# Performance work log

Hardware: AMD Instinct MI355X
Metric: run time of the kernel (lower is better)

Reference implementation:

```python
import jax, jax.numpy as jnp
import numpy as np

EMB_D, N_SLOTS, KEY_D, N_ITER = 768, 8, 128, 5
ATTN_EPS = 1e-8
LN_EPS = 1e-5


def layer_norm(x, g, b):
    mu = jnp.mean(x, axis=-1, keepdims=True)
    var = jnp.mean(jnp.square(x - mu), axis=-1, keepdims=True)
    return (x - mu) * jax.lax.rsqrt(var + LN_EPS) * g + b


def xavier(key, shape):
    fan_in, fan_out = shape[-1], shape[-2] if len(shape) > 1 else shape[-1]
    a = float(np.sqrt(6.0 / (fan_in + fan_out)))
    return jax.random.uniform(key, shape, jnp.float32, -a, a)


def setup_inputs() -> dict:
    key = jax.random.key(0)
    ks = jax.random.split(key, 24)
    B, N = 128, 196
    k = KEY_D
    inp = {
        "features": jax.random.normal(ks[0], (B, N, EMB_D), jnp.float32),
        "slot_noise": jax.random.normal(ks[1], (B, N_SLOTS, k), jnp.float32),
        # LayerNorms
        "ln_in_g": jnp.ones((EMB_D,), jnp.float32), "ln_in_b": jnp.zeros((EMB_D,), jnp.float32),
        "ln_slot_g": jnp.ones((k,), jnp.float32), "ln_slot_b": jnp.zeros((k,), jnp.float32),
        "ln_out_g": jnp.ones((k,), jnp.float32), "ln_out_b": jnp.zeros((k,), jnp.float32),
        "ln_dec_g": jnp.ones((k,), jnp.float32), "ln_dec_b": jnp.zeros((k,), jnp.float32),
        # slot prior
        "mu": xavier(ks[2], (1, 1, k)),
        "log_sigma": xavier(ks[3], (1, 1, k)),
        # projections (torch Linear weight layout: [out, in])
        "Wk": xavier(ks[4], (k, EMB_D)),
        "Wq": xavier(ks[5], (k, k)),
        "Wv": xavier(ks[6], (k, EMB_D)),
        # GRUCell
        "W_ih": jax.random.uniform(ks[7], (3 * k, k), jnp.float32, -1.0/np.sqrt(k), 1.0/np.sqrt(k)),
        "W_hh": jax.random.uniform(ks[8], (3 * k, k), jnp.float32, -1.0/np.sqrt(k), 1.0/np.sqrt(k)),
        "b_ih": jnp.zeros((3 * k,), jnp.float32),
        "b_hh": jnp.zeros((3 * k,), jnp.float32),
        # slot MLP
        "mlp_W1": xavier(ks[9], (k, k)), "mlp_b1": jnp.zeros((k,), jnp.float32),
        "mlp_W2": xavier(ks[10], (k, k)), "mlp_b2": jnp.zeros((k,), jnp.float32),
        # decoder
        "dec_W1": xavier(ks[11], (2 * k, k)), "dec_b1": jnp.zeros((2 * k,), jnp.float32),
        "dec_W2": xavier(ks[12], (EMB_D, 2 * k)), "dec_b2": jnp.zeros((EMB_D,), jnp.float32),
        "dec_W3": xavier(ks[13], (EMB_D, EMB_D)), "dec_b3": jnp.zeros((EMB_D,), jnp.float32),
    }
    return inp


def gru_cell(x, h, W_ih, W_hh, b_ih, b_hh):
    gi = x @ W_ih.T + b_ih  # [*, 3k]
    gh = h @ W_hh.T + b_hh
    ir, iz, inn = jnp.split(gi, 3, axis=-1)
    hr, hz, hn = jnp.split(gh, 3, axis=-1)
    r = jax.nn.sigmoid(ir + hr)
    z = jax.nn.sigmoid(iz + hz)
    n = jnp.tanh(inn + r * hn)
    return (1.0 - z) * n + z * h


def reference(features, slot_noise, ln_in_g, ln_in_b, ln_slot_g, ln_slot_b,
              ln_out_g, ln_out_b, ln_dec_g, ln_dec_b, mu, log_sigma,
              Wk, Wq, Wv, W_ih, W_hh, b_ih, b_hh,
              mlp_W1, mlp_b1, mlp_W2, mlp_b2,
              dec_W1, dec_b1, dec_W2, dec_b2, dec_W3, dec_b3):
    feats_ln = layer_norm(features, ln_in_g, ln_in_b)  # [B,N,E]
    slots = slot_noise * jnp.exp(log_sigma) + mu       # [B,K,D]
    k_proj = (feats_ln @ Wk.T) * (KEY_D ** -0.5)       # [B,N,D]
    v_proj = feats_ln @ Wv.T                           # [B,N,D]

    attn_vis = None
    for _ in range(N_ITER):
        slots_prev = slots
        s_ln = layer_norm(slots, ln_slot_g, ln_slot_b)
        q = s_ln @ Wq.T                                # [B,K,D]
        logits = jnp.einsum('bnd,bkd->bnk', k_proj, q)
        attn_vis = jax.nn.softmax(logits, axis=-1)     # softmax over slots
        attn = attn_vis + ATTN_EPS
        attn = attn / jnp.sum(attn, axis=-2, keepdims=True)  # normalize over tokens
        updates = jnp.einsum('bnk,bnd->bkd', attn, v_proj)
        slots = gru_cell(updates, slots_prev, W_ih, W_hh, b_ih, b_hh)
        h = jax.nn.relu(layer_norm(slots, ln_out_g, ln_out_b) @ mlp_W1.T + mlp_b1)
        slots = slots + (h @ mlp_W2.T + mlp_b2)

    sf = layer_norm(slots, ln_dec_g, ln_dec_b)
    sf = jax.nn.relu(sf @ dec_W1.T + dec_b1)
    sf = jax.nn.relu(sf @ dec_W2.T + dec_b2)
    sf = sf @ dec_W3.T + dec_b3                        # [B,K,E]
    recon = jnp.einsum('bkd,bnk->bnd', sf, attn_vis)   # [B,N,E]
    recon_loss = jnp.mean(jnp.square(recon - features))
    return slots, attn_vis, recon_loss
```

## Files before the change

kernel.cpp:

```cpp
#include <hip/hip_runtime.h>
#include <hip/hip_bf16.h>
#include <math.h>

#define B_    128
#define N_    196
#define E_    768
#define K_    8
#define D_    128
#define BNR   (B_*N_)
#define ITERS 5

#define OFF_PART   0
#define OFF_SDEC   512
#define OFF_WBF    66048
#define OFF_KPBF   639488
#define OFF_VPTBF  2343424
#define OFF_ABF    4178432

typedef __attribute__((ext_vector_type(8))) short bf16x8;
typedef __attribute__((ext_vector_type(4))) float f32x4;

#define MFMA16(a, b, c) __builtin_amdgcn_mfma_f32_16x16x32_bf16(a, b, c, 0, 0, 0)

__device__ __forceinline__ float wave_red_sum64(float v) {
    #pragma unroll
    for (int o = 32; o > 0; o >>= 1) v += __shfl_xor(v, o);
    return v;
}

__device__ __forceinline__ unsigned short f2bf(float v) {
    union { float f; unsigned int u; } c; c.f = v;
    unsigned int u = c.u + 0x7fffu + ((c.u >> 16) & 1u);
    return (unsigned short)(u >> 16);
}

__device__ __forceinline__ void gl_lds16(const void* g, void* l) {
    __builtin_amdgcn_global_load_lds(
        (const __attribute__((address_space(1))) unsigned int*)g,
        (__attribute__((address_space(3))) unsigned int*)l, 16, 0, 0);
}

__device__ __forceinline__ int swz128(int row, int j) {
    return row * 128 + ((((j >> 3) ^ (row & 7))) << 3) + (j & 7);
}
__device__ __forceinline__ int swz256(int row, int j) {
    return row * 256 + ((((j >> 3) ^ (row & 7))) << 3) + (j & 7);
}
__device__ __forceinline__ bf16x8 ldA128(const unsigned short* base, int row, int kq, int ks) {
    int ch = (ks * 4 + kq) ^ (row & 7);
    return *(const bf16x8*)(base + row * 128 + ch * 8);
}
__device__ __forceinline__ bf16x8 ldA256(const unsigned short* base, int row, int kq, int ks) {
    int ch = (ks * 4 + kq) ^ (row & 7);
    return *(const bf16x8*)(base + row * 256 + ch * 8);
}
__device__ __forceinline__ bf16x8 ldW128(const unsigned short* W, int row, int ks, int kq) {
    return *(const bf16x8*)(W + (size_t)row * 128 + ks * 32 + kq * 8);
}

__global__ __launch_bounds__(256) void wfold_k(const float* __restrict__ Wq,
                                               const float* __restrict__ Wk,
                                               unsigned short* __restrict__ WMt) {
    __shared__ __align__(16) unsigned short Aq[128 * 128];
    __shared__ __align__(16) unsigned short Bk[128 * 128];
    const float s = 0.08838834764831845f;
    int t = threadIdx.x;
    int e0 = blockIdx.x * 128;
    for (int idx = t; idx < 16384; idx += 256) {
        int o = idx >> 7, c = idx & 127;
        Aq[swz128(c, o)] = f2bf(Wq[(size_t)o * 128 + c]);
        Bk[swz128(c, o)] = f2bf(Wk[(size_t)o * 768 + e0 + c] * s);
    }
    __syncthreads();
    int w = t >> 6, l = t & 63;
    int wr = w >> 1, wc = w & 1, fr = l & 15, kq = l >> 4;
    f32x4 acc[4][4];
    #pragma unroll
    for (int mi = 0; mi < 4; ++mi)
        #pragma unroll
        for (int nj = 0; nj < 4; ++nj) acc[mi][nj] = (f32x4){0.f, 0.f, 0.f, 0.f};
    #pragma unroll
    for (int ks = 0; ks < 4; ++ks) {
        bf16x8 af[4], bfr[4];
        #pragma unroll
        for (int mi = 0; mi < 4; ++mi) af[mi] = ldA128(Aq, wr * 64 + mi * 16 + fr, kq, ks);
        #pragma unroll
        for (int nj = 0; nj < 4; ++nj) bfr[nj] = ldA128(Bk, wc * 64 + nj * 16 + fr, kq, ks);
        #pragma unroll
        for (int mi = 0; mi < 4; ++mi)
            #pragma unroll
            for (int nj = 0; nj < 4; ++nj)
                acc[mi][nj] = MFMA16(af[mi], bfr[nj], acc[mi][nj]);
    }
    #pragma unroll
    for (int mi = 0; mi < 4; ++mi) {
        int rowbase = wr * 64 + mi * 16 + kq * 4;
        #pragma unroll
        for (int nj = 0; nj < 4; ++nj) {
            int col = e0 + wc * 64 + nj * 16 + fr;
            #pragma unroll
            for (int r = 0; r < 4; ++r)
                WMt[(size_t)(rowbase + r) * 768 + col] = f2bf(acc[mi][nj][r]);
        }
    }
}

struct WCEnt { const float* s; unsigned short* d; int t0; };
struct WCArgs { WCEnt m[8]; };

__global__ __launch_bounds__(256) void wprep_k(WCArgs a,
                                               unsigned short* __restrict__ kpb,
                                               unsigned short* __restrict__ vpt) {
    int bid = blockIdx.x;
    if (bid < 512) {
        int i = 0;
        #pragma unroll
        for (int j = 1; j < 8; ++j) if (bid >= a.m[j].t0) i = j;
        int off = (bid - a.m[i].t0) * 2048 + threadIdx.x * 8;
        const float* s = a.m[i].s + off;
        unsigned short* d = a.m[i].d + off;
        float4 v0 = *(const float4*)s, v1 = *(const float4*)(s + 4);
        ushort4 o0, o1;
        o0.x = f2bf(v0.x); o0.y = f2bf(v0.y); o0.z = f2bf(v0.z); o0.w = f2bf(v0.w);
        o1.x = f2bf(v1.x); o1.y = f2bf(v1.y); o1.z = f2bf(v1.z); o1.w = f2bf(v1.w);
        *(ushort4*)d = o0; *(ushort4*)(d + 4) = o1;
    } else {
        int i = (bid - 512) * 256 + threadIdx.x;
        ushort4 z = {0, 0, 0, 0};
        if (i < 49152) {
            int q = i * 4;
            int b = q / 1536, off = q - b * 1536;
            *(ushort4*)(kpb + ((size_t)b * 208 + 196) * 128 + off) = z;
        } else {
            int c = i - 49152;
            int bd = c / 7, cc = c - bd * 7;
            *(ushort4*)(vpt + (size_t)bd * 224 + 196 + cc * 4) = z;
        }
    }
}

__global__ __launch_bounds__(256) void ln_bf16_k(const float* __restrict__ f,
                                                 const float* __restrict__ g,
                                                 const float* __restrict__ bv,
                                                 unsigned short* __restrict__ out) {
    int wid = blockIdx.x * 4 + (threadIdx.x >> 6);
    int lane = threadIdx.x & 63;
    const float* row = f + (size_t)wid * E_;
    float4 x[3];
    float s = 0.f, s2 = 0.f;
    #pragma unroll
    for (int c = 0; c < 3; ++c) {
        x[c] = *(const float4*)(row + c * 256 + lane * 4);
        s  += x[c].x + x[c].y + x[c].z + x[c].w;
        s2 += x[c].x * x[c].x + x[c].y * x[c].y + x[c].z * x[c].z + x[c].w * x[c].w;
    }
    s  = wave_red_sum64(s);
    s2 = wave_red_sum64(s2);
    float m = s * (1.f / E_);
    float rs = rsqrtf(s2 * (1.f / E_) - m * m + 1e-5f);
    #pragma unroll
    for (int c = 0; c < 3; ++c) {
        float4 g4 = *(const float4*)(g + c * 256 + lane * 4);
        float4 b4 = *(const float4*)(bv + c * 256 + lane * 4);
        ushort4 o;
        o.x = f2bf((x[c].x - m) * rs * g4.x + b4.x);
        o.y = f2bf((x[c].y - m) * rs * g4.y + b4.y);
        o.z = f2bf((x[c].z - m) * rs * g4.z + b4.z);
        o.w = f2bf((x[c].w - m) * rs * g4.w + b4.w);
        *(ushort4*)(out + (size_t)wid * E_ + c * 256 + lane * 4) = o;
    }
}

__global__ __launch_bounds__(512) void mfma_proj_k(const unsigned short* __restrict__ Abf,
                                                   const unsigned short* __restrict__ WMt,
                                                   const unsigned short* __restrict__ Wv_bf,
                                                   unsigned short* __restrict__ kpq_bf,
                                                   unsigned short* __restrict__ vpT_bf) {
    __shared__ __align__(16) unsigned short As[128 * 64];
    __shared__ __align__(16) unsigned short Bs[256 * 64];
    const int t = threadIdx.x, w = t >> 6, l = t & 63;
    const int m0 = blockIdx.x * 128;
    const int wr = w >> 2, wc = w & 3;
    const int fr = l & 15, kq = l >> 4;
    f32x4 acc[4][4];
    #pragma unroll
    for (int mi = 0; mi < 4; ++mi)
        #pragma unroll
        for (int nj = 0; nj < 4; ++nj) acc[mi][nj] = (f32x4){0.f, 0.f, 0.f, 0.f};

    for (int ks = 0; ks < E_; ks += 64) {
        __syncthreads();
        #pragma unroll
        for (int j = 0; j < 2; ++j) {
            int ci = j * 512 + (w << 6) + l;
            int r = ci >> 3, c = ci & 7, cg = c ^ (r & 7);
            gl_lds16(Abf + (size_t)(m0 + r) * E_ + ks + cg * 8,
                     As + (size_t)(j * 512 + (w << 6)) * 8);
        }
        #pragma unroll
        for (int j = 0; j < 4; ++j) {
            int ci = j * 512 + (w << 6) + l;
            int r = ci >> 3, c = ci & 7, cg = c ^ (r & 7);
            const unsigned short* src = (r < 128)
                ? WMt   + (size_t)r * E_ + ks + cg * 8
                : Wv_bf + (size_t)(r - 128) * E_ + ks + cg * 8;
            gl_lds16(src, Bs + (size_t)(j * 512 + (w << 6)) * 8);
        }
        __syncthreads();
        #pragma unroll
        for (int kk = 0; kk < 2; ++kk) {
            bf16x8 af[4], bfr[4];
            #pragma unroll
            for (int mi = 0; mi < 4; ++mi) {
                int rr = wr * 64 + mi * 16 + fr;
                af[mi] = *(const bf16x8*)(As + rr * 64 + (((kk * 4 + kq) ^ (rr & 7))) * 8);
            }
            #pragma unroll
            for (int nj = 0; nj < 4; ++nj) {
                int rr = wc * 64 + nj * 16 + fr;
                bfr[nj] = *(const bf16x8*)(Bs + rr * 64 + (((kk * 4 + kq) ^ (rr & 7))) * 8);
            }
            #pragma unroll
            for (int mi = 0; mi < 4; ++mi)
                #pragma unroll
                for (int nj = 0; nj < 4; ++nj)
                    acc[mi][nj] = MFMA16(af[mi], bfr[nj], acc[mi][nj]);
        }
    }
    __syncthreads();
    if (wc < 2) {
        #pragma unroll
        for (int mi = 0; mi < 4; ++mi) {
            int rowbase = m0 + wr * 64 + mi * 16 + kq * 4;
            #pragma unroll
            for (int r = 0; r < 4; ++r) {
                int m = rowbase + r;
                int b = m / 196, rr = m - b * 196;
                size_t o = ((size_t)b * 208 + rr) * 128;
                #pragma unroll
                for (int nj = 0; nj < 4; ++nj)
                    kpq_bf[o + wc * 64 + nj * 16 + fr] = f2bf(acc[mi][nj][r]);
            }
        }
    } else {
        int dbase = (wc - 2) * 64;
        #pragma unroll
        for (int mi = 0; mi < 4; ++mi) {
            int tok = wr * 64 + mi * 16 + kq * 4;
            #pragma unroll
            for (int nj = 0; nj < 4; ++nj) {
                int d = dbase + nj * 16 + fr;
                ushort4 pk;
                pk.x = f2bf(acc[mi][nj][0]); pk.y = f2bf(acc[mi][nj][1]);
                pk.z = f2bf(acc[mi][nj][2]); pk.w = f2bf(acc[mi][nj][3]);
                *(ushort4*)(Bs + d * 128 + (tok ^ ((d & 7) << 3))) = pk;
            }
        }
    }
    __syncthreads();
    {
        int d = t >> 2, mg = t & 3;
        #pragma unroll
        for (int sc = 0; sc < 4; ++sc) {
            int mstart = mg * 32 + sc * 8;
            int cm = mstart >> 3;
            const unsigned short* src = Bs + d * 128 + ((cm ^ (d & 7)) << 3);
            int g0 = m0 + mstart;
            int b0 = g0 / 196, rr0 = g0 - b0 * 196;
            int b7 = (g0 + 7) / 196;
            if (b0 == b7) {
                unsigned short* dst = vpT_bf + ((size_t)b0 * 128 + d) * 224 + rr0;
                *(ushort4*)(dst)     = *(const ushort4*)(src);
                *(ushort4*)(dst + 4) = *(const ushort4*)(src + 4);
            } else {
                #pragma unroll
                for (int e = 0; e < 8; ++e) {
                    int g = g0 + e;
                    int bb = g / 196, rr = g - bb * 196;
                    vpT_bf[((size_t)bb * 128 + d) * 224 + rr] = src[e];
                }
            }
        }
    }
}

template<int KTOT, int EPI>
__global__ __launch_bounds__(256) void mfma_mlp_k(const unsigned short* __restrict__ A,
                                                  const unsigned short* __restrict__ Bw,
                                                  const float* __restrict__ bias,
                                                  unsigned short* __restrict__ out_bf,
                                                  float* __restrict__ out_f,
                                                  int ldN) {
    __shared__ __align__(16) unsigned short As[128 * 64];
    __shared__ __align__(16) unsigned short Bs[128 * 64];
    const int t = threadIdx.x, w = t >> 6, l = t & 63;
    const int m0 = blockIdx.x * 128;
    const int n0 = blockIdx.y * 128;
    const int wr = w >> 1, wc = w & 1;
    const int fr = l & 15, kq = l >> 4;
    f32x4 acc[4][4];
    #pragma unroll
    for (int mi = 0; mi < 4; ++mi)
        #pragma unroll
        for (int nj = 0; nj < 4; ++nj) acc[mi][nj] = (f32x4){0.f, 0.f, 0.f, 0.f};

    for (int ks = 0; ks < KTOT; ks += 64) {
        __syncthreads();
        #pragma unroll
        for (int j = 0; j < 4; ++j) {
            int ci = (w << 8) + (j << 6) + l;
            int r = ci >> 3, c = ci & 7;
            int cg = c ^ (r & 7);
            gl_lds16(A  + (size_t)(m0 + r) * KTOT + ks + cg * 8,
                     As + (size_t)((w << 8) + (j << 6)) * 8);
            gl_lds16(Bw + (size_t)(n0 + r) * KTOT + ks + cg * 8,
                     Bs + (size_t)((w << 8) + (j << 6)) * 8);
        }
        __syncthreads();
        #pragma unroll
        for (int kk = 0; kk < 2; ++kk) {
            bf16x8 af[4], bfr[4];
            int ch = (kk * 4 + kq) ^ (fr & 7);
            #pragma unroll
            for (int mi = 0; mi < 4; ++mi)
                af[mi] = *(const bf16x8*)(As + (wr * 64 + mi * 16 + fr) * 64 + ch * 8);
            #pragma unroll
            for (int nj = 0; nj < 4; ++nj)
                bfr[nj] = *(const bf16x8*)(Bs + (wc * 64 + nj * 16 + fr) * 64 + ch * 8);
            #pragma unroll
            for (int mi = 0; mi < 4; ++mi)
                #pragma unroll
                for (int nj = 0; nj < 4; ++nj)
                    acc[mi][nj] = MFMA16(af[mi], bfr[nj], acc[mi][nj]);
        }
    }
    #pragma unroll
    for (int mi = 0; mi < 4; ++mi) {
        int rowbase = m0 + wr * 64 + mi * 16 + kq * 4;
        #pragma unroll
        for (int nj = 0; nj < 4; ++nj) {
            int col = n0 + wc * 64 + nj * 16 + fr;
            float bc = bias[col];
            #pragma unroll
            for (int r = 0; r < 4; ++r) {
                float v = acc[mi][nj][r] + bc;
                if (EPI == 0)
                    out_bf[(size_t)(rowbase + r) * ldN + col] = f2bf(fmaxf(v, 0.f));
                else
                    out_f[(size_t)(rowbase + r) * ldN + col] = v;
            }
        }
    }
}

__global__ __launch_bounds__(512) void slot_iter_mfma(
    const float* __restrict__ noise,
    const float* __restrict__ lsg, const float* __restrict__ lsb,
    const float* __restrict__ log_, const float* __restrict__ lob,
    const float* __restrict__ ldg_, const float* __restrict__ ldb_,
    const float* __restrict__ mup, const float* __restrict__ lsig,
    const unsigned short* __restrict__ Wih_bf,
    const unsigned short* __restrict__ Whh_bf,
    const float* __restrict__ bih, const float* __restrict__ bhh,
    const unsigned short* __restrict__ W1_bf, const float* __restrict__ mb1,
    const unsigned short* __restrict__ W2_bf, const float* __restrict__ mb2,
    const unsigned short* __restrict__ kpq_bf,
    const unsigned short* __restrict__ vpT_bf,
    float* __restrict__ out_slots, float* __restrict__ out_attn,
    unsigned short* __restrict__ sdec_bf) {

    __shared__ float slots[8][128];
    __shared__ float attn[208][9];
    __shared__ float colpart[8][8];
    __shared__ __align__(16) unsigned short sln_bf[2048];
    __shared__ __align__(16) unsigned short upd_bf[2048];
    __shared__ __align__(16) unsigned short slots_bf[2048];
    __shared__ __align__(16) unsigned short h_bf[2048];
    __shared__ __align__(16) unsigned short attnT_bf[4096];

    const int b = blockIdx.x, t = threadIdx.x;
    const int lane = t & 63, w = t >> 6;
    const int fr = lane & 15, kq = lane >> 4;

    for (int i = t; i < 2048; i += 512) {
        sln_bf[i] = 0; upd_bf[i] = 0; slots_bf[i] = 0; h_bf[i] = 0;
    }
    for (int i = t; i < 4096; i += 512) attnT_bf[i] = 0;

    for (int idx = t; idx < 1024; idx += 512) {
        int k = idx >> 7, d = idx & 127;
        float v = noise[(size_t)b * 1024 + idx] * expf(lsig[d]) + mup[d];
        slots[k][d] = v;
        slots_bf[swz128(k, d)] = f2bf(v);
    }
    __syncthreads();

    for (int it = 0; it < ITERS; ++it) {
        bool last = (it == ITERS - 1);
        {
            float x0 = slots[w][lane], x1 = slots[w][lane + 64];
            float s  = wave_red_sum64(x0 + x1);
            float s2 = wave_red_sum64(x0 * x0 + x1 * x1);
            float m = s * 0.0078125f;
            float rs = rsqrtf(s2 * 0.0078125f - m * m + 1e-5f);
            sln_bf[swz128(w, lane)]      = f2bf((x0 - m) * rs * lsg[lane]      + lsb[lane]);
            sln_bf[swz128(w, lane + 64)] = f2bf((x1 - m) * rs * lsg[lane + 64] + lsb[lane + 64]);
        }
        __syncthreads();
        {
            float cp = 0.f;
            #pragma unroll
            for (int p = 0; p < 2; ++p) {
                int tt = w + p * 8;
                if (tt <= 12) {
                    f32x4 acc = {0.f, 0.f, 0.f, 0.f};
                    const unsigned short* kpr = kpq_bf + ((size_t)b * 208 + tt * 16 + fr) * 128;
                    #pragma unroll
                    for (int ks = 0; ks < 4; ++ks)
                        acc = MFMA16(*(const bf16x8*)(kpr + ks * 32 + kq * 8),
                                     ldA128(sln_bf, fr, kq, ks), acc);
                    #pragma unroll
                    for (int r = 0; r < 4; ++r) {
                        float v = acc[r];
                        float mx = fmaxf(v, __shfl_xor(v, 1));
                        mx = fmaxf(mx, __shfl_xor(mx, 2));
                        mx = fmaxf(mx, __shfl_xor(mx, 4));
                        float e = expf(v - mx);
                        float sm = e;
                        sm += __shfl_xor(sm, 1); sm += __shfl_xor(sm, 2); sm += __shfl_xor(sm, 4);
                        float a = e / sm;
                        int tok = tt * 16 + kq * 4 + r;
                        bool valid = (tok < 196);
                        if (fr < 8 && valid) attn[tok][fr] = a;
                        cp += valid ? a : 0.f;
                    }
                }
            }
            cp += __shfl_xor(cp, 16);
            cp += __shfl_xor(cp, 32);
            if (lane < 8) colpart[w][lane] = cp;
        }
        __syncthreads();
        {
            int k = t & 7;
            float cs = colpart[0][k] + colpart[1][k] + colpart[2][k] + colpart[3][k]
                     + colpart[4][k] + colpart[5][k] + colpart[6][k] + colpart[7][k]
                     + 196.0f * 1e-8f;
            float inv = 1.f / cs;
            for (int idx = t; idx < 1568; idx += 512) {
                int n = idx >> 3;
                float raw = attn[n][k];
                attnT_bf[swz256(k, n)] = f2bf((raw + 1e-8f) * inv);
                if (last) out_attn[((size_t)b * 196 + n) * 8 + k] = raw;
            }
        }
        __syncthreads();
        {
            f32x4 acc = {0.f, 0.f, 0.f, 0.f};
            const unsigned short* vpr = vpT_bf + ((size_t)b * 128 + w * 16 + fr) * 224;
            #pragma unroll
            for (int ks = 0; ks < 7; ++ks)
                acc = MFMA16(ldA256(attnT_bf, fr, kq, ks),
                             *(const bf16x8*)(vpr + ks * 32 + kq * 8), acc);
            if (kq < 2) {
                #pragma unroll
                for (int r = 0; r < 4; ++r)
                    upd_bf[swz128(kq * 4 + r, w * 16 + fr)] = f2bf(acc[r]);
            }
        }
        __syncthreads();
        {
            f32x4 gi0 = {0,0,0,0}, gi1 = {0,0,0,0}, gi2 = {0,0,0,0};
            f32x4 gh0 = {0,0,0,0}, gh1 = {0,0,0,0}, gh2 = {0,0,0,0};
            #pragma unroll
            for (int ks = 0; ks < 4; ++ks) {
                bf16x8 au = ldA128(upd_bf,   fr, kq, ks);
                bf16x8 as = ldA128(slots_bf, fr, kq, ks);
                gi0 = MFMA16(au, ldW128(Wih_bf,       w * 16 + fr, ks, kq), gi0);
                gi1 = MFMA16(au, ldW128(Wih_bf, 128 + w * 16 + fr, ks, kq), gi1);
                gi2 = MFMA16(au, ldW128(Wih_bf, 256 + w * 16 + fr, ks, kq), gi2);
                gh0 = MFMA16(as, ldW128(Whh_bf,       w * 16 + fr, ks, kq), gh0);
                gh1 = MFMA16(as, ldW128(Whh_bf, 128 + w * 16 + fr, ks, kq), gh1);
                gh2 = MFMA16(as, ldW128(Whh_bf, 256 + w * 16 + fr, ks, kq), gh2);
            }
            if (kq < 2) {
                int d = w * 16 + fr;
                float bi0 = bih[d], bi1 = bih[128 + d], bi2 = bih[256 + d];
                float bh0 = bhh[d], bh1 = bhh[128 + d], bh2 = bhh[256 + d];
                #pragma unroll
                for (int r = 0; r < 4; ++r) {
                    int m = kq * 4 + r;
                    float rr = 1.f / (1.f + expf(-((gi0[r] + bi0) + (gh0[r] + bh0))));
                    float zz = 1.f / (1.f + expf(-((gi1[r] + bi1) + (gh1[r] + bh1))));
                    float nn = tanhf((gi2[r] + bi2) + rr * (gh2[r] + bh2));
                    float h = slots[m][d];
                    slots[m][d] = (1.f - zz) * nn + zz * h;
                }
            }
        }
        __syncthreads();
        {
            float x0 = slots[w][lane], x1 = slots[w][lane + 64];
            float s  = wave_red_sum64(x0 + x1);
            float s2 = wave_red_sum64(x0 * x0 + x1 * x1);
            float m = s * 0.0078125f;
            float rs = rsqrtf(s2 * 0.0078125f - m * m + 1e-5f);
            sln_bf[swz128(w, lane)]      = f2bf((x0 - m) * rs * log_[lane]      + lob[lane]);
            sln_bf[swz128(w, lane + 64)] = f2bf((x1 - m) * rs * log_[lane + 64] + lob[lane + 64]);
        }
        __syncthreads();
        {
            f32x4 acc = {0.f, 0.f, 0.f, 0.f};
            #pragma unroll
            for (int ks = 0; ks < 4; ++ks)
                acc = MFMA16(ldA128(sln_bf, fr, kq, ks), ldW128(W1_bf, w * 16 + fr, ks, kq), acc);
            if (kq < 2) {
                float b1 = mb1[w * 16 + fr];
                #pragma unroll
                for (int r = 0; r < 4; ++r)
                    h_bf[swz128(kq * 4 + r, w * 16 + fr)] = f2bf(fmaxf(acc[r] + b1, 0.f));
            }
        }
        __syncthreads();
        {
            f32x4 acc = {0.f, 0.f, 0.f, 0.f};
            #pragma unroll
            for (int ks = 0; ks < 4; ++ks)
                acc = MFMA16(ldA128(h_bf, fr, kq, ks), ldW128(W2_bf, w * 16 + fr, ks, kq), acc);
            if (kq < 2) {
                float b2 = mb2[w * 16 + fr];
                #pragma unroll
                for (int r = 0; r < 4; ++r) {
                    int m = kq * 4 + r, d = w * 16 + fr;
                    float v = slots[m][d] + acc[r] + b2;
                    slots[m][d] = v;
                    slots_bf[swz128(m, d)] = f2bf(v);
                }
            }
        }
        __syncthreads();
    }
    {
        float x0 = slots[w][lane], x1 = slots[w][lane + 64];
        out_slots[(size_t)b * 1024 + w * 128 + lane]      = x0;
        out_slots[(size_t)b * 1024 + w * 128 + lane + 64] = x1;
        float s  = wave_red_sum64(x0 + x1);
        float s2 = wave_red_sum64(x0 * x0 + x1 * x1);
        float m = s * 0.0078125f;
        float rs = rsqrtf(s2 * 0.0078125f - m * m + 1e-5f);
        sdec_bf[((size_t)b * 8 + w) * 128 + lane]      = f2bf((x0 - m) * rs * ldg_[lane]      + ldb_[lane]);
        sdec_bf[((size_t)b * 8 + w) * 128 + lane + 64] = f2bf((x1 - m) * rs * ldg_[lane + 64] + ldb_[lane + 64]);
    }
}

__global__ __launch_bounds__(256) void recon_loss_k(
    const float* __restrict__ feats, const float* __restrict__ attnv,
    const float* __restrict__ sf, float* __restrict__ partials) {

    __shared__ float sfl[8][768];
    __shared__ float al[49][8];
    __shared__ float wred[4];
    int b = blockIdx.x, qd = blockIdx.y, t = threadIdx.x;
    for (int idx = t; idx < 8 * 768; idx += 256)
        ((float*)sfl)[idx] = sf[(size_t)b * 8 * 768 + idx];
    int n0 = qd * 49;
    for (int idx = t; idx < 49 * 8; idx += 256)
        ((float*)al)[idx] = attnv[((size_t)b * N_ + n0) * 8 + idx];
    __syncthreads();
    float acc = 0.f;
    for (int nl = 0; nl < 49; ++nl) {
        float a0 = al[nl][0], a1 = al[nl][1], a2 = al[nl][2], a3 = al[nl][3];
        float a4 = al[nl][4], a5 = al[nl][5], a6 = al[nl][6], a7 = al[nl][7];
        const float* frow = feats + ((size_t)(b * N_ + n0 + nl)) * E_;
        for (int c = t; c < E_; c += 256) {
            float r = sfl[0][c]*a0 + sfl[1][c]*a1 + sfl[2][c]*a2 + sfl[3][c]*a3
                    + sfl[4][c]*a4 + sfl[5][c]*a5 + sfl[6][c]*a6 + sfl[7][c]*a7;
            float d = r - frow[c];
            acc += d * d;
        }
    }
    acc = wave_red_sum64(acc);
    int lane = t & 63, w = t >> 6;
    if (lane == 0) wred[w] = acc;
    __syncthreads();
    if (t == 0) partials[b * 4 + qd] = wred[0] + wred[1] + wred[2] + wred[3];
}

__global__ __launch_bounds__(512) void loss_final_k(const float* __restrict__ partials,
                                                    float* __restrict__ out) {
    __shared__ float wred[8];
    int t = threadIdx.x;
    float v = partials[t];
    v = wave_red_sum64(v);
    if ((t & 63) == 0) wred[t >> 6] = v;
    __syncthreads();
    if (t == 0) {
        float s = 0.f;
        #pragma unroll
        for (int i = 0; i < 8; ++i) s += wred[i];
        out[0] = s / (float)(B_ * N_ * E_);
    }
}

extern "C" void kernel_launch(void* const* d_in, const int* in_sizes, int n_in,
                              void* d_out, int out_size, void* d_ws, size_t ws_size,
                              hipStream_t stream) {
    (void)in_sizes; (void)n_in; (void)out_size; (void)ws_size;
    const float* feats     = (const float*)d_in[0];
    const float* noise     = (const float*)d_in[1];
    const float* ln_in_g   = (const float*)d_in[2];
    const float* ln_in_b   = (const float*)d_in[3];
    const float* ln_slot_g = (const float*)d_in[4];
    const float* ln_slot_b = (const float*)d_in[5];
    const float* ln_out_g  = (const float*)d_in[6];
    const float* ln_out_b  = (const float*)d_in[7];
    const float* ln_dec_g  = (const float*)d_in[8];
    const float* ln_dec_b  = (const float*)d_in[9];
    const float* mu        = (const float*)d_in[10];
    const float* log_sigma = (const float*)d_in[11];
    const float* Wk        = (const float*)d_in[12];
    const float* Wq        = (const float*)d_in[13];
    const float* Wv        = (const float*)d_in[14];
    const float* W_ih      = (const float*)d_in[15];
    const float* W_hh      = (const float*)d_in[16];
    const float* b_ih      = (const float*)d_in[17];
    const float* b_hh      = (const float*)d_in[18];
    const float* mlp_W1    = (const float*)d_in[19];
    const float* mlp_b1    = (const float*)d_in[20];
    const float* mlp_W2    = (const float*)d_in[21];
    const float* mlp_b2    = (const float*)d_in[22];
    const float* dec_W1    = (const float*)d_in[23];
    const float* dec_b1    = (const float*)d_in[24];
    const float* dec_W2    = (const float*)d_in[25];
    const float* dec_b2    = (const float*)d_in[26];
    const float* dec_W3    = (const float*)d_in[27];
    const float* dec_b3    = (const float*)d_in[28];

    float* ws    = (float*)d_ws;
    float* parts = ws + OFF_PART;
    unsigned short* sdec_bf = (unsigned short*)(ws + OFF_SDEC);
    unsigned short* Wbase   = (unsigned short*)(ws + OFF_WBF);
    unsigned short* Wv_bf   = Wbase;
    unsigned short* Wih_bf  = Wbase + 98304;
    unsigned short* Whh_bf  = Wbase + 147456;
    unsigned short* W1_bf   = Wbase + 196608;
    unsigned short* W2_bf   = Wbase + 212992;
    unsigned short* dW1_bf  = Wbase + 229376;
    unsigned short* dW2_bf  = Wbase + 262144;
    unsigned short* dW3_bf  = Wbase + 458752;
    unsigned short* WMt     = Wbase + 1048576;
    unsigned short* kpq_bf  = (unsigned short*)(ws + OFF_KPBF);
    unsigned short* vpT_bf  = (unsigned short*)(ws + OFF_VPTBF);
    unsigned short* Abf     = (unsigned short*)(ws + OFF_ABF);
    float*          sf      = ws + OFF_ABF;
    unsigned short* h1_bf   = (unsigned short*)(ws + OFF_ABF + 786432);
    unsigned short* h2_bf   = (unsigned short*)(ws + OFF_ABF + 786432 + 131072);

    float* out_slots = (float*)d_out;
    float* out_attn  = out_slots + 131072;
    float* out_loss  = out_slots + 331776;

    wfold_k<<<6, 256, 0, stream>>>(Wq, Wk, WMt);

    WCArgs wa;
    wa.m[0] = {Wv,     Wv_bf,  0};
    wa.m[1] = {W_ih,   Wih_bf, 48};
    wa.m[2] = {W_hh,   Whh_bf, 72};
    wa.m[3] = {mlp_W1, W1_bf,  96};
    wa.m[4] = {mlp_W2, W2_bf,  104};
    wa.m[5] = {dec_W1, dW1_bf, 112};
    wa.m[6] = {dec_W2, dW2_bf, 128};
    wa.m[7] = {dec_W3, dW3_bf, 224};
    wprep_k<<<1152, 256, 0, stream>>>(wa, kpq_bf, vpT_bf);

    ln_bf16_k<<<BNR / 4, 256, 0, stream>>>(feats, ln_in_g, ln_in_b, Abf);
    mfma_proj_k<<<BNR / 128, 512, 0, stream>>>(Abf, WMt, Wv_bf, kpq_bf, vpT_bf);

    slot_iter_mfma<<<B_, 512, 0, stream>>>(noise, ln_slot_g, ln_slot_b, ln_out_g, ln_out_b,
                                           ln_dec_g, ln_dec_b, mu, log_sigma,
                                           Wih_bf, Whh_bf, b_ih, b_hh,
                                           W1_bf, mlp_b1, W2_bf, mlp_b2, kpq_bf, vpT_bf,
                                           out_slots, out_attn, sdec_bf);

    mfma_mlp_k<128, 0><<<dim3(8, 2), 256, 0, stream>>>(sdec_bf, dW1_bf, dec_b1, h1_bf, nullptr, 256);
    mfma_mlp_k<256, 0><<<dim3(8, 6), 256, 0, stream>>>(h1_bf,  dW2_bf, dec_b2, h2_bf, nullptr, 768);
    mfma_mlp_k<768, 1><<<dim3(8, 6), 256, 0, stream>>>(h2_bf,  dW3_bf, dec_b3, nullptr, sf, 768);

    recon_loss_k<<<dim3(B_, 4), 256, 0, stream>>>(feats, out_attn, sf, parts);
    loss_final_k<<<1, 512, 0, stream>>>(parts, out_loss);
}
```

Measured before the change: 199.2 us.

## Merge weight-prep kernels, keep slot-iteration operands in registers, fold token normalization

```diff
diff --git a/kernel.cpp b/kernel.cpp
--- a/kernel.cpp
+++ b/kernel.cpp
@@ -58,65 +58,64 @@
     return *(const bf16x8*)(W + (size_t)row * 128 + ks * 32 + kq * 8);
 }
 
-__global__ __launch_bounds__(256) void wfold_k(const float* __restrict__ Wq,
-                                               const float* __restrict__ Wk,
-                                               unsigned short* __restrict__ WMt) {
+struct WCEnt { const float* s; unsigned short* d; int t0; };
+struct WCArgs { WCEnt m[8]; };
+
+__global__ __launch_bounds__(256) void prep_all_k(const float* __restrict__ Wq,
+                                                  const float* __restrict__ Wk,
+                                                  unsigned short* __restrict__ WMt,
+                                                  WCArgs a,
+                                                  unsigned short* __restrict__ kpb,
+                                                  unsigned short* __restrict__ vpt) {
     __shared__ __align__(16) unsigned short Aq[128 * 128];
     __shared__ __align__(16) unsigned short Bk[128 * 128];
-    const float s = 0.08838834764831845f;
+    int bid = blockIdx.x;
     int t = threadIdx.x;
-    int e0 = blockIdx.x * 128;
-    for (int idx = t; idx < 16384; idx += 256) {
-        int o = idx >> 7, c = idx & 127;
-        Aq[swz128(c, o)] = f2bf(Wq[(size_t)o * 128 + c]);
-        Bk[swz128(c, o)] = f2bf(Wk[(size_t)o * 768 + e0 + c] * s);
-    }
-    __syncthreads();
-    int w = t >> 6, l = t & 63;
-    int wr = w >> 1, wc = w & 1, fr = l & 15, kq = l >> 4;
-    f32x4 acc[4][4];
-    #pragma unroll
-    for (int mi = 0; mi < 4; ++mi)
-        #pragma unroll
-        for (int nj = 0; nj < 4; ++nj) acc[mi][nj] = (f32x4){0.f, 0.f, 0.f, 0.f};
-    #pragma unroll
-    for (int ks = 0; ks < 4; ++ks) {
-        bf16x8 af[4], bfr[4];
-        #pragma unroll
-        for (int mi = 0; mi < 4; ++mi) af[mi] = ldA128(Aq, wr * 64 + mi * 16 + fr, kq, ks);
-        #pragma unroll
-        for (int nj = 0; nj < 4; ++nj) bfr[nj] = ldA128(Bk, wc * 64 + nj * 16 + fr, kq, ks);
+    if (bid < 6) {
+        const float s = 0.08838834764831845f;
+        int e0 = bid * 128;
+        for (int idx = t; idx < 16384; idx += 256) {
+            int o = idx >> 7, c = idx & 127;
+            Aq[swz128(c, o)] = f2bf(Wq[(size_t)o * 128 + c]);
+            Bk[swz128(c, o)] = f2bf(Wk[(size_t)o * 768 + e0 + c] * s);
+        }
+        __syncthreads();
+        int w = t >> 6, l = t & 63;
+        int wr = w >> 1, wc = w & 1, fr = l & 15, kq = l >> 4;
+        f32x4 acc[4][4];
         #pragma unroll
         for (int mi = 0; mi < 4; ++mi)
             #pragma unroll
-            for (int nj = 0; nj < 4; ++nj)
-                acc[mi][nj] = MFMA16(af[mi], bfr[nj], acc[mi][nj]);
-    }
-    #pragma unroll
-    for (int mi = 0; mi < 4; ++mi) {
-        int rowbase = wr * 64 + mi * 16 + kq * 4;
-        #pragma unroll
-        for (int nj = 0; nj < 4; ++nj) {
-            int col = e0 + wc * 64 + nj * 16 + fr;
-            #pragma unroll
-            for (int r = 0; r < 4; ++r)
-                WMt[(size_t)(rowbase + r) * 768 + col] = f2bf(acc[mi][nj][r]);
-        }
-    }
-}
-
-struct WCEnt { const float* s; unsigned short* d; int t0; };
-struct WCArgs { WCEnt m[8]; };
-
-__global__ __launch_bounds__(256) void wprep_k(WCArgs a,
-                                               unsigned short* __restrict__ kpb,
-                                               unsigned short* __restrict__ vpt) {
-    int bid = blockIdx.x;
-    if (bid < 512) {
-        int i = 0;
-        #pragma unroll
-        for (int j = 1; j < 8; ++j) if (bid >= a.m[j].t0) i = j;
-        int off = (bid - a.m[i].t0) * 2048 + threadIdx.x * 8;
+            for (int nj = 0; nj < 4; ++nj) acc[mi][nj] = (f32x4){0.f, 0.f, 0.f, 0.f};
+        #pragma unroll
+        for (int ks = 0; ks < 4; ++ks) {
+            bf16x8 af[4], bfr[4];
+            #pragma unroll
+            for (int mi = 0; mi < 4; ++mi) af[mi] = ldA128(Aq, wr * 64 + mi * 16 + fr, kq, ks);
+            #pragma unroll
+            for (int nj = 0; nj < 4; ++nj) bfr[nj] = ldA128(Bk, wc * 64 + nj * 16 + fr, kq, ks);
+            #pragma unroll
+            for (int mi = 0; mi < 4; ++mi)
+                #pragma unroll
+                for (int nj = 0; nj < 4; ++nj)
+                    acc[mi][nj] = MFMA16(af[mi], bfr[nj], acc[mi][nj]);
+        }
+        #pragma unroll
+        for (int mi = 0; mi < 4; ++mi) {
+            int rowbase = wr * 64 + mi * 16 + kq * 4;
+            #pragma unroll
+            for (int nj = 0; nj < 4; ++nj) {
+                int col = e0 + wc * 64 + nj * 16 + fr;
+                #pragma unroll
+                for (int r = 0; r < 4; ++r)
+                    WMt[(size_t)(rowbase + r) * 768 + col] = f2bf(acc[mi][nj][r]);
+            }
+        }
+    } else if (bid < 518) {
+        int cbid = bid - 6, i = 0;
+        #pragma unroll
+        for (int j = 1; j < 8; ++j) if (cbid >= a.m[j].t0) i = j;
+        int off = (cbid - a.m[i].t0) * 2048 + t * 8;
         const float* s = a.m[i].s + off;
         unsigned short* d = a.m[i].d + off;
         float4 v0 = *(const float4*)s, v1 = *(const float4*)(s + 4);
@@ -125,7 +124,7 @@
         o1.x = f2bf(v1.x); o1.y = f2bf(v1.y); o1.z = f2bf(v1.z); o1.w = f2bf(v1.w);
         *(ushort4*)d = o0; *(ushort4*)(d + 4) = o1;
     } else {
-        int i = (bid - 512) * 256 + threadIdx.x;
+        int i = (bid - 518) * 256 + t;
         ushort4 z = {0, 0, 0, 0};
         if (i < 49152) {
             int q = i * 4;
@@ -370,7 +369,6 @@
     unsigned short* __restrict__ sdec_bf) {
 
     __shared__ float slots[8][128];
-    __shared__ float attn[208][9];
     __shared__ float colpart[8][8];
     __shared__ __align__(16) unsigned short sln_bf[2048];
     __shared__ __align__(16) unsigned short upd_bf[2048];
@@ -392,6 +390,35 @@
         float v = noise[(size_t)b * 1024 + idx] * expf(lsig[d]) + mup[d];
         slots[k][d] = v;
         slots_bf[swz128(k, d)] = f2bf(v);
+    }
+
+    bf16x8 kpq_r[2][4];
+    #pragma unroll
+    for (int p = 0; p < 2; ++p)
+        #pragma unroll
+        for (int ks = 0; ks < 4; ++ks) kpq_r[p][ks] = (bf16x8){0,0,0,0,0,0,0,0};
+    #pragma unroll
+    for (int p = 0; p < 2; ++p) {
+        int tt = w + p * 8;
+        if (tt <= 12) {
+            const unsigned short* kpr = kpq_bf + ((size_t)b * 208 + tt * 16 + fr) * 128;
+            #pragma unroll
+            for (int ks = 0; ks < 4; ++ks)
+                kpq_r[p][ks] = *(const bf16x8*)(kpr + ks * 32 + kq * 8);
+        }
+    }
+    bf16x8 vpt_r[7];
+    {
+        const unsigned short* vpr = vpT_bf + ((size_t)b * 128 + w * 16 + fr) * 224;
+        #pragma unroll
+        for (int ks = 0; ks < 7; ++ks)
+            vpt_r[ks] = *(const bf16x8*)(vpr + ks * 32 + kq * 8);
+    }
+    bf16x8 w1_r[4], w2_r[4];
+    #pragma unroll
+    for (int ks = 0; ks < 4; ++ks) {
+        w1_r[ks] = ldW128(W1_bf, w * 16 + fr, ks, kq);
+        w2_r[ks] = ldW128(W2_bf, w * 16 + fr, ks, kq);
     }
     __syncthreads();
 
@@ -414,11 +441,9 @@
                 int tt = w + p * 8;
                 if (tt <= 12) {
                     f32x4 acc = {0.f, 0.f, 0.f, 0.f};
-                    const unsigned short* kpr = kpq_bf + ((size_t)b * 208 + tt * 16 + fr) * 128;
                     #pragma unroll
                     for (int ks = 0; ks < 4; ++ks)
-                        acc = MFMA16(*(const bf16x8*)(kpr + ks * 32 + kq * 8),
-                                     ldA128(sln_bf, fr, kq, ks), acc);
+                        acc = MFMA16(kpq_r[p][ks], ldA128(sln_bf, fr, kq, ks), acc);
                     #pragma unroll
                     for (int r = 0; r < 4; ++r) {
                         float v = acc[r];
@@ -431,7 +456,10 @@
                         float a = e / sm;
                         int tok = tt * 16 + kq * 4 + r;
                         bool valid = (tok < 196);
-                        if (fr < 8 && valid) attn[tok][fr] = a;
+                        if (fr < 8 && valid) {
+                            attnT_bf[swz256(fr, tok)] = f2bf(a);
+                            if (last) out_attn[((size_t)b * 196 + tok) * 8 + fr] = a;
+                        }
                         cp += valid ? a : 0.f;
                     }
                 }
@@ -442,30 +470,19 @@
         }
         __syncthreads();
         {
-            int k = t & 7;
-            float cs = colpart[0][k] + colpart[1][k] + colpart[2][k] + colpart[3][k]
-                     + colpart[4][k] + colpart[5][k] + colpart[6][k] + colpart[7][k]
-                     + 196.0f * 1e-8f;
-            float inv = 1.f / cs;
-            for (int idx = t; idx < 1568; idx += 512) {
-                int n = idx >> 3;
-                float raw = attn[n][k];
-                attnT_bf[swz256(k, n)] = f2bf((raw + 1e-8f) * inv);
-                if (last) out_attn[((size_t)b * 196 + n) * 8 + k] = raw;
-            }
-        }
-        __syncthreads();
-        {
             f32x4 acc = {0.f, 0.f, 0.f, 0.f};
-            const unsigned short* vpr = vpT_bf + ((size_t)b * 128 + w * 16 + fr) * 224;
             #pragma unroll
             for (int ks = 0; ks < 7; ++ks)
-                acc = MFMA16(ldA256(attnT_bf, fr, kq, ks),
-                             *(const bf16x8*)(vpr + ks * 32 + kq * 8), acc);
+                acc = MFMA16(ldA256(attnT_bf, fr, kq, ks), vpt_r[ks], acc);
             if (kq < 2) {
                 #pragma unroll
-                for (int r = 0; r < 4; ++r)
-                    upd_bf[swz128(kq * 4 + r, w * 16 + fr)] = f2bf(acc[r]);
+                for (int r = 0; r < 4; ++r) {
+                    int k = kq * 4 + r;
+                    float cs = colpart[0][k] + colpart[1][k] + colpart[2][k] + colpart[3][k]
+                             + colpart[4][k] + colpart[5][k] + colpart[6][k] + colpart[7][k]
+                             + 196.0f * 1e-8f;
+                    upd_bf[swz128(k, w * 16 + fr)] = f2bf(acc[r] / cs);
+                }
             }
         }
         __syncthreads();
@@ -513,7 +530,7 @@
             f32x4 acc = {0.f, 0.f, 0.f, 0.f};
             #pragma unroll
             for (int ks = 0; ks < 4; ++ks)
-                acc = MFMA16(ldA128(sln_bf, fr, kq, ks), ldW128(W1_bf, w * 16 + fr, ks, kq), acc);
+                acc = MFMA16(ldA128(sln_bf, fr, kq, ks), w1_r[ks], acc);
             if (kq < 2) {
                 float b1 = mb1[w * 16 + fr];
                 #pragma unroll
@@ -526,7 +543,7 @@
             f32x4 acc = {0.f, 0.f, 0.f, 0.f};
             #pragma unroll
             for (int ks = 0; ks < 4; ++ks)
-                acc = MFMA16(ldA128(h_bf, fr, kq, ks), ldW128(W2_bf, w * 16 + fr, ks, kq), acc);
+                acc = MFMA16(ldA128(h_bf, fr, kq, ks), w2_r[ks], acc);
             if (kq < 2) {
                 float b2 = mb2[w * 16 + fr];
                 #pragma unroll
@@ -660,8 +677,6 @@
     float* out_attn  = out_slots + 131072;
     float* out_loss  = out_slots + 331776;
 
-    wfold_k<<<6, 256, 0, stream>>>(Wq, Wk, WMt);
-
     WCArgs wa;
     wa.m[0] = {Wv,     Wv_bf,  0};
     wa.m[1] = {W_ih,   Wih_bf, 48};
@@ -671,7 +686,7 @@
     wa.m[5] = {dec_W1, dW1_bf, 112};
     wa.m[6] = {dec_W2, dW2_bf, 128};
     wa.m[7] = {dec_W3, dW3_bf, 224};
-    wprep_k<<<1152, 256, 0, stream>>>(wa, kpq_bf, vpT_bf);
+    prep_all_k<<<1158, 256, 0, stream>>>(Wq, Wk, WMt, wa, kpq_bf, vpT_bf);
 
     ln_bf16_k<<<BNR / 4, 256, 0, stream>>>(feats, ln_in_g, ln_in_b, Abf);
     mfma_proj_k<<<BNR / 128, 512, 0, stream>>>(Abf, WMt, Wv_bf, kpq_bf, vpT_bf);
```

Result: slower. 206.1 us (+3.5%).
